# Kernel tuning notes

Measured on AMD Instinct MI355X. Metric: run time of the kernel, lower is better.

## Reference

```python
import jax, jax.numpy as jnp
import numpy as np

BANDS, ROWS, SIM_THRESH = 16, 8, 0.5


def setup_inputs() -> dict:
    key = jax.random.key(0)
    k1, k2 = jax.random.split(key)
    N, D = 8192, 256
    Z = jax.random.normal(k1, (N, D), dtype=jnp.float32)
    # random hyperplanes ~ N(0, I), (bands*rows, D) -- sampled once (torch samples in forward)
    planes = jax.random.normal(k2, (BANDS * ROWS, D), dtype=jnp.float32)
    return {"Z": Z, "planes": planes}


def reference(Z, planes):
    N, D = Z.shape
    # signature: sign of projections, (bands, rows, N); +/-1 vs bool is equivalent for bucketing
    sig_bits = (planes @ Z.T >= 0).reshape(BANDS, ROWS, N)
    # bit-pack each band's row-signature into an integer key == hashing the signature bytes
    bit_weights = (2 ** jnp.arange(ROWS)).astype(jnp.int32)
    keys = jnp.einsum('brn,r->bn', sig_bits.astype(jnp.int32), bit_weights)  # (bands, N)
    # cosine pairwise similarity (row-normalized GEMM)
    Zn = Z / jnp.linalg.norm(Z, axis=1, keepdims=True)
    sim = Zn @ Zn.T  # (N, N)
    # number of bands in which i and j fall in the same LSH bucket
    def band_match(acc, k):
        return acc + (k[:, None] == k[None, :]).astype(jnp.float32), None
    counts, _ = jax.lax.scan(band_match, jnp.zeros((N, N), jnp.float32), keys)
    # original masks the diagonal with -inf, thresholds at sim_thresh, and emits one
    # (sim) entry per matching band into an uncoalesced sparse tensor; densified this
    # is counts * sim on surviving off-diagonal pairs.
    mask = (sim >= SIM_THRESH) & (~jnp.eye(N, dtype=bool))
    return jnp.where(mask, counts * sim, 0.0)
```

## Files before the change

### kernel.cpp

```cpp
#include <hip/hip_runtime.h>

typedef __attribute__((ext_vector_type(4))) float floatx4;

#define N_PTS 8192
#define D_DIM 256
#define N_PLANES 128
#define NTILE 64

__device__ inline int zbytes(unsigned int w) {
    unsigned int t = ((w & 0x7f7f7f7fu) + 0x7f7f7f7fu) | w | 0x7f7f7f7fu;
    return __popc(~t);
}

__device__ inline void load_lds16(const void* g, void* l) {
    __builtin_amdgcn_global_load_lds(
        (const __attribute__((address_space(1))) unsigned int*)g,
        (__attribute__((address_space(3))) unsigned int*)l, 16, 0, 0);
}

__global__ __launch_bounds__(256) void keys_norm_fill_kernel(
    const float* __restrict__ Z, const float* __restrict__ planes,
    unsigned int* __restrict__ keys4, unsigned char* __restrict__ Zn,
    float* __restrict__ out) {
    __shared__ __align__(16) float zs[16][D_DIM];
    int t = threadIdx.x;
    int base = blockIdx.x * 16;

    floatx4 z4 = {0.f, 0.f, 0.f, 0.f};
    floatx4* outv = (floatx4*)out + (size_t)blockIdx.x * 32768 + t;

    const float4* zsrc = (const float4*)(Z + (size_t)base * D_DIM);
    float4* zdst = (float4*)&zs[0][0];
#pragma unroll
    for (int i = 0; i < 4; ++i) zdst[t + i * 256] = zsrc[t + i * 256];
    __syncthreads();

    {
        int row = t >> 4, ch = t & 15;
        const float* zr = &zs[row][ch * 16];
        float ss = 0.f;
#pragma unroll
        for (int i = 0; i < 16; ++i) ss += zr[i] * zr[i];
#pragma unroll
        for (int off = 8; off > 0; off >>= 1) ss += __shfl_xor(ss, off);
        float inv = rsqrtf(ss);
        int4 o;
#pragma unroll
        for (int q = 0; q < 4; ++q) {
            int p = __builtin_amdgcn_cvt_pk_fp8_f32(zr[q * 4] * inv,
                                                    zr[q * 4 + 1] * inv, 0, false);
            p = __builtin_amdgcn_cvt_pk_fp8_f32(zr[q * 4 + 2] * inv,
                                                zr[q * 4 + 3] * inv, p, true);
            ((int*)&o)[q] = p;
        }
        *(int4*)(Zn + (size_t)(base + row) * D_DIM + ch * 16) = o;
    }

    int p = t & 127;
    int hf = t >> 7;
    int wave = t >> 6, lane = t & 63;
    const float4* pr = (const float4*)(planes + (size_t)p * D_DIM);

    float acc[8] = {};
    for (int kk = 0; kk < D_DIM / 4; ++kk) {
        __builtin_nontemporal_store(z4, outv + (size_t)(2 * kk) * 256);
        __builtin_nontemporal_store(z4, outv + (size_t)(2 * kk + 1) * 256);
        float4 pv = pr[kk];
#pragma unroll
        for (int j = 0; j < 8; ++j) {
            float4 zv = *(const float4*)&zs[hf * 8 + j][kk * 4];
            acc[j] += pv.x * zv.x + pv.y * zv.y + pv.z * zv.z + pv.w * zv.w;
        }
    }

#pragma unroll
    for (int j = 0; j < 8; ++j) {
        unsigned long long mask = __ballot(acc[j] >= 0.0f);
        if (lane < 2) {
            keys4[(size_t)(base + hf * 8 + j) * 4 + (wave & 1) * 2 + lane] =
                (unsigned int)(mask >> (32 * lane));
        }
    }
}

__global__ __launch_bounds__(256, 4) void gemm_kernel(
    const unsigned char* __restrict__ Zn, const uint4* __restrict__ keys,
    float* __restrict__ out) {
    __shared__ __align__(16) unsigned char As[16384];
    __shared__ __align__(16) unsigned char Bs[16384];
    __shared__ uint4 krow[128];
    __shared__ uint4 kcol[128];

    int idx = blockIdx.x;
    int bi = (int)((129.0f - sqrtf(16641.0f - 8.0f * (float)idx)) * 0.5f);
    while ((bi + 1) * NTILE - ((bi + 1) * bi) / 2 <= idx) ++bi;
    while (bi * NTILE - (bi * (bi - 1)) / 2 > idx) --bi;
    int bj = bi + (idx - (bi * NTILE - (bi * (bi - 1)) / 2));
    int rowBase = bi * 128;
    int colBase = bj * 128;
    bool diag = (bi == bj);

    int t = threadIdx.x;
    if (t < 128)
        krow[t] = keys[rowBase + t];
    else
        kcol[t - 128] = keys[colBase + (t - 128)];

    const unsigned char* ZnA = Zn + (size_t)rowBase * D_DIM;
    const unsigned char* ZnB = Zn + (size_t)colBase * D_DIM;

    int wave = t >> 6, lane = t & 63;
    int wm = wave >> 1, wn = wave & 1;
    int quad = lane >> 4, l16 = lane & 15;

    floatx4 acc[4][4] = {};

    for (int s = 0; s < 2; ++s) {
        __syncthreads();
#pragma unroll
        for (int i = 0; i < 4; ++i) {
            int sa = i * 256 + t;
            int c = sa >> 7, row = sa & 127;
            size_t gOff = (size_t)row * D_DIM + s * 128 + c * 16;
            load_lds16(ZnA + gOff, &As[sa * 16]);
            load_lds16(ZnB + gOff, &Bs[sa * 16]);
        }
        __syncthreads();

#pragma unroll
        for (int k2 = 0; k2 < 4; ++k2) {
            int kByte = k2 * 32 + quad * 8;
            int cc = kByte >> 4;
            int off8 = kByte & 8;
            long afr[4], bfr[4];
#pragma unroll
            for (int mt = 0; mt < 4; ++mt)
                afr[mt] = *(const long*)&As[(cc * 128 + wm * 64 + mt * 16 + l16) * 16 + off8];
#pragma unroll
            for (int nt = 0; nt < 4; ++nt)
                bfr[nt] = *(const long*)&Bs[(cc * 128 + wn * 64 + nt * 16 + l16) * 16 + off8];
#pragma unroll
            for (int mt = 0; mt < 4; ++mt)
#pragma unroll
                for (int nt = 0; nt < 4; ++nt)
                    acc[mt][nt] = __builtin_amdgcn_mfma_f32_16x16x32_fp8_fp8(
                        afr[mt], bfr[nt], acc[mt][nt], 0, 0, 0);
        }
    }

    bool any = false;
#pragma unroll
    for (int mt = 0; mt < 4; ++mt)
#pragma unroll
        for (int nt = 0; nt < 4; ++nt)
#pragma unroll
            for (int r = 0; r < 4; ++r) {
                int gi = rowBase + wm * 64 + mt * 16 + quad * 4 + r;
                int gj = colBase + wn * 64 + nt * 16 + l16;
                any = any || (acc[mt][nt][r] >= 0.5f && gi != gj);
            }

    if (__ballot(any)) {
#pragma unroll
        for (int mt = 0; mt < 4; ++mt)
#pragma unroll
            for (int nt = 0; nt < 4; ++nt) {
                int lj = wn * 64 + nt * 16 + l16;
                int gj = colBase + lj;
                uint4 kj = kcol[lj];
#pragma unroll
                for (int r = 0; r < 4; ++r) {
                    int liL = wm * 64 + mt * 16 + quad * 4 + r;
                    int gi = rowBase + liL;
                    float s = acc[mt][nt][r];
                    if (s >= 0.5f && gi != gj) {
                        uint4 ki = krow[liL];
                        int c = zbytes(ki.x ^ kj.x) + zbytes(ki.y ^ kj.y) +
                                zbytes(ki.z ^ kj.z) + zbytes(ki.w ^ kj.w);
                        float v = s * (float)c;
                        out[(size_t)gi * N_PTS + gj] = v;
                        if (!diag) out[(size_t)gj * N_PTS + gi] = v;
                    }
                }
            }
    }
}

extern "C" void kernel_launch(void* const* d_in, const int* in_sizes, int n_in,
                              void* d_out, int out_size, void* d_ws,
                              size_t ws_size, hipStream_t stream) {
    const float* Z = (const float*)d_in[0];
    const float* planes = (const float*)d_in[1];
    float* out = (float*)d_out;

    unsigned char* Zn = (unsigned char*)d_ws;
    unsigned int* keys4 =
        (unsigned int*)((char*)d_ws + (size_t)N_PTS * D_DIM);

    keys_norm_fill_kernel<<<N_PTS / 16, 256, 0, stream>>>(Z, planes, keys4, Zn,
                                                          out);
    int nblocks = NTILE * (NTILE + 1) / 2;
    gemm_kernel<<<nblocks, 256, 0, stream>>>(Zn, (const uint4*)keys4, out);
}
```

Baseline: 292.3 us.

## Compute LSH keys with per-row split-K dot products and shuffle reductions

Reworks the key/normalize kernel so each group of 16 threads holds one Z row in registers, dropping the shared-memory staging and the block barrier. Each plane projection becomes a split-K dot product over 16 lanes, reduced with xor shuffles, and the signature bits are packed into per-row words. The output zero-fill stores are interleaved with the plane loop. This trades LDS traffic for many more shuffle reductions and redundant plane loads per thread group.

After: 361.8 us. +23.8%, slower.

```diff
diff --git a/kernel.cpp b/kernel.cpp
--- a/kernel.cpp
+++ b/kernel.cpp
@@ -18,68 +18,64 @@
         (__attribute__((address_space(3))) unsigned int*)l, 16, 0, 0);
 }
 
+__device__ inline float dot4(float4 a, float4 b) {
+    return a.x * b.x + a.y * b.y + a.z * b.z + a.w * b.w;
+}
+
 __global__ __launch_bounds__(256) void keys_norm_fill_kernel(
     const float* __restrict__ Z, const float* __restrict__ planes,
     unsigned int* __restrict__ keys4, unsigned char* __restrict__ Zn,
     float* __restrict__ out) {
-    __shared__ __align__(16) float zs[16][D_DIM];
     int t = threadIdx.x;
     int base = blockIdx.x * 16;
+    int row = t >> 4, ch = t & 15;
 
     floatx4 z4 = {0.f, 0.f, 0.f, 0.f};
     floatx4* outv = (floatx4*)out + (size_t)blockIdx.x * 32768 + t;
 
-    const float4* zsrc = (const float4*)(Z + (size_t)base * D_DIM);
-    float4* zdst = (float4*)&zs[0][0];
-#pragma unroll
-    for (int i = 0; i < 4; ++i) zdst[t + i * 256] = zsrc[t + i * 256];
-    __syncthreads();
+    const float4* zp = (const float4*)(Z + (size_t)(base + row) * D_DIM + ch * 16);
+    float4 z0 = zp[0], z1 = zp[1], z2 = zp[2], z3 = zp[3];
 
     {
-        int row = t >> 4, ch = t & 15;
-        const float* zr = &zs[row][ch * 16];
-        float ss = 0.f;
-#pragma unroll
-        for (int i = 0; i < 16; ++i) ss += zr[i] * zr[i];
+        float ss = dot4(z0, z0) + dot4(z1, z1) + dot4(z2, z2) + dot4(z3, z3);
 #pragma unroll
         for (int off = 8; off > 0; off >>= 1) ss += __shfl_xor(ss, off);
         float inv = rsqrtf(ss);
         int4 o;
-#pragma unroll
-        for (int q = 0; q < 4; ++q) {
-            int p = __builtin_amdgcn_cvt_pk_fp8_f32(zr[q * 4] * inv,
-                                                    zr[q * 4 + 1] * inv, 0, false);
-            p = __builtin_amdgcn_cvt_pk_fp8_f32(zr[q * 4 + 2] * inv,
-                                                zr[q * 4 + 3] * inv, p, true);
-            ((int*)&o)[q] = p;
+        int p;
+        p = __builtin_amdgcn_cvt_pk_fp8_f32(z0.x * inv, z0.y * inv, 0, false);
+        o.x = __builtin_amdgcn_cvt_pk_fp8_f32(z0.z * inv, z0.w * inv, p, true);
+        p = __builtin_amdgcn_cvt_pk_fp8_f32(z1.x * inv, z1.y * inv, 0, false);
+        o.y = __builtin_amdgcn_cvt_pk_fp8_f32(z1.z * inv, z1.w * inv, p, true);
+        p = __builtin_amdgcn_cvt_pk_fp8_f32(z2.x * inv, z2.y * inv, 0, false);
+        o.z = __builtin_amdgcn_cvt_pk_fp8_f32(z2.z * inv, z2.w * inv, p, true);
+        p = __builtin_amdgcn_cvt_pk_fp8_f32(z3.x * inv, z3.y * inv, 0, false);
+        o.w = __builtin_amdgcn_cvt_pk_fp8_f32(z3.z * inv, z3.w * inv, p, true);
+        *(int4*)(Zn + (size_t)(base + row) * D_DIM + ch * 16) = o;
+    }
+
+    unsigned int kw[4];
+#pragma unroll
+    for (int w = 0; w < 4; ++w) {
+        unsigned int acc = 0u;
+#pragma unroll 4
+        for (int pb = 0; pb < 32; ++pb) {
+            int p = w * 32 + pb;
+            __builtin_nontemporal_store(z4, outv + (size_t)p * 256);
+            const float4* pp =
+                (const float4*)(planes + (size_t)p * D_DIM + ch * 16);
+            float4 a = pp[0], b = pp[1], c = pp[2], d = pp[3];
+            float dp = dot4(a, z0) + dot4(b, z1) + dot4(c, z2) + dot4(d, z3);
+#pragma unroll
+            for (int off = 8; off > 0; off >>= 1) dp += __shfl_xor(dp, off);
+            acc |= (dp >= 0.0f ? 1u : 0u) << pb;
         }
-        *(int4*)(Zn + (size_t)(base + row) * D_DIM + ch * 16) = o;
-    }
-
-    int p = t & 127;
-    int hf = t >> 7;
-    int wave = t >> 6, lane = t & 63;
-    const float4* pr = (const float4*)(planes + (size_t)p * D_DIM);
-
-    float acc[8] = {};
-    for (int kk = 0; kk < D_DIM / 4; ++kk) {
-        __builtin_nontemporal_store(z4, outv + (size_t)(2 * kk) * 256);
-        __builtin_nontemporal_store(z4, outv + (size_t)(2 * kk + 1) * 256);
-        float4 pv = pr[kk];
-#pragma unroll
-        for (int j = 0; j < 8; ++j) {
-            float4 zv = *(const float4*)&zs[hf * 8 + j][kk * 4];
-            acc[j] += pv.x * zv.x + pv.y * zv.y + pv.z * zv.z + pv.w * zv.w;
-        }
-    }
-
-#pragma unroll
-    for (int j = 0; j < 8; ++j) {
-        unsigned long long mask = __ballot(acc[j] >= 0.0f);
-        if (lane < 2) {
-            keys4[(size_t)(base + hf * 8 + j) * 4 + (wave & 1) * 2 + lane] =
-                (unsigned int)(mask >> (32 * lane));
-        }
+        kw[w] = acc;
+    }
+    if (ch == 0) {
+        uint4 k;
+        k.x = kw[0]; k.y = kw[1]; k.z = kw[2]; k.w = kw[3];
+        ((uint4*)keys4)[base + row] = k;
     }
 }
 
```
